# Kernel optimization log

Hardware: AMD Instinct MI355X
Metric: run time of the kernel (lower is better)

Reference implementation:

```python
import jax, jax.numpy as jnp
import numpy as np
from jax import lax

B, L, IN_DIM, D_MODEL = 4, 4096, 256, 512
EXPAND, D_STATE, D_CONV = 2, 16, 4
D_INNER = EXPAND * D_MODEL              # 1024
DT_RANK = (D_MODEL + 15) // 16          # 32 (mamba default: ceil(d_model/16))


def setup_inputs() -> dict:
    key = jax.random.key(0)
    ks = jax.random.split(key, 12)
    s = 0.02
    x = jax.random.normal(ks[0], (B, L, IN_DIM), dtype=jnp.float32)
    # input_proj: nn.Linear(input_dim, d_model) with bias
    w_proj = jax.random.normal(ks[1], (IN_DIM, D_MODEL), dtype=jnp.float32) * s
    b_proj = jnp.zeros((D_MODEL,), dtype=jnp.float32)
    # Mamba in_proj: Linear(d_model, 2*d_inner, bias=False)
    in_w = jax.random.normal(ks[2], (D_MODEL, 2 * D_INNER), dtype=jnp.float32) * s
    # depthwise causal conv1d: weight (d_inner, d_conv), bias (d_inner,)
    conv_w = jax.random.normal(ks[3], (D_INNER, D_CONV), dtype=jnp.float32) * s
    conv_b = jnp.zeros((D_INNER,), dtype=jnp.float32)
    # x_proj: Linear(d_inner, dt_rank + 2*d_state, bias=False)
    xproj_w = jax.random.normal(ks[4], (D_INNER, DT_RANK + 2 * D_STATE), dtype=jnp.float32) * s
    # dt_proj: Linear(dt_rank, d_inner) with bias
    dt_w = jax.random.normal(ks[5], (DT_RANK, D_INNER), dtype=jnp.float32) * s
    dt_b = jax.random.normal(ks[6], (D_INNER,), dtype=jnp.float32) * 0.1
    # A_log init: log(1..d_state) broadcast over d_inner (mamba S4D-real init)
    A_log = jnp.log(jnp.broadcast_to(jnp.arange(1, D_STATE + 1, dtype=jnp.float32), (D_INNER, D_STATE)))
    D_skip = jnp.ones((D_INNER,), dtype=jnp.float32)
    # out_proj: Linear(d_inner, d_model, bias=False)
    out_w = jax.random.normal(ks[7], (D_INNER, D_MODEL), dtype=jnp.float32) * s
    return {"x": x, "w_proj": w_proj, "b_proj": b_proj, "in_w": in_w,
            "conv_w": conv_w, "conv_b": conv_b, "xproj_w": xproj_w,
            "dt_w": dt_w, "dt_b": dt_b, "A_log": A_log, "D_skip": D_skip,
            "out_w": out_w}


def _mamba_forward(x, w_proj, b_proj, in_w, conv_w, conv_b, xproj_w,
                   dt_w, dt_b, A_log, D_skip, out_w):
    silu = jax.nn.silu
    # input projection: [B,L,IN_DIM] -> [B,L,D_MODEL]
    h = x @ w_proj + b_proj
    # in_proj -> split into x-branch and gate z: each [B,L,D_INNER]
    xz = h @ in_w
    u, z = jnp.split(xz, 2, axis=-1)
    # depthwise causal conv1d over L
    u_c = jnp.transpose(u, (0, 2, 1))                       # [B,E,L]
    u_c = jnp.pad(u_c, ((0, 0), (0, 0), (D_CONV - 1, 0)))   # causal left-pad
    u_c = lax.conv_general_dilated(
        u_c, conv_w[:, None, :], window_strides=(1,), padding='VALID',
        dimension_numbers=('NCH', 'OIH', 'NCH'), feature_group_count=D_INNER)
    u = silu(jnp.transpose(u_c, (0, 2, 1)) + conv_b)         # [B,L,E]
    # input-dependent dt, B, C
    x_dbl = u @ xproj_w                                      # [B,L,dt_rank+2N]
    dt, Bm, Cm = jnp.split(x_dbl, [DT_RANK, DT_RANK + D_STATE], axis=-1)
    dt = jax.nn.softplus(dt @ dt_w + dt_b)                   # [B,L,E]
    A = -jnp.exp(A_log)                                      # [E,N]
    # selective scan over time (carry h: [B,E,N])
    def step(hs, inp):
        dt_t, B_t, C_t, u_t = inp                            # (B,E),(B,N),(B,N),(B,E)
        dA = jnp.exp(dt_t[..., None] * A)                    # [B,E,N]
        hs = dA * hs + (dt_t * u_t)[..., None] * B_t[:, None, :]
        y_t = jnp.einsum('ben,bn->be', hs, C_t)
        return hs, y_t
    xs = (jnp.transpose(dt, (1, 0, 2)), jnp.transpose(Bm, (1, 0, 2)),
          jnp.transpose(Cm, (1, 0, 2)), jnp.transpose(u, (1, 0, 2)))
    h0 = jnp.zeros((B, D_INNER, D_STATE), dtype=u.dtype)
    _, ys = lax.scan(step, h0, xs)                           # [L,B,E]
    y = jnp.transpose(ys, (1, 0, 2)) + u * D_skip            # [B,L,E]
    y = y * silu(z)
    out = y @ out_w                                          # [B,L,D_MODEL]
    return out.mean(axis=1)                                  # [B,D_MODEL]


def reference(x, w_proj, b_proj, in_w, conv_w, conv_b, xproj_w,
              dt_w, dt_b, A_log, D_skip, out_w):
    return _mamba_forward(x, w_proj, b_proj, in_w, conv_w, conv_b, xproj_w,
                          dt_w, dt_b, A_log, D_skip, out_w)
```

## Files before the change

### kernel.cpp

```cpp
#include <hip/hip_runtime.h>
#include <cstdint>
#include <cstddef>


#define B_    4
#define L_    4096
#define M_    (B_ * L_)
#define DIN   256
#define DM    512
#define DI    1024
#define NS    16
#define RK    32
#define XD    64
#define TCH   64
#define NCH   (L_ / TCH)
#define NCHAN (B_ * DI)

#define L2E   1.44269504088896f
#define LN2   0.69314718055995f

typedef __bf16 bf16_t;
typedef bf16_t bf16x8 __attribute__((ext_vector_type(8)));
typedef float  f32x4  __attribute__((ext_vector_type(4)));

static __device__ __forceinline__ float fexp2(float x)  { return __builtin_amdgcn_exp2f(x); }
static __device__ __forceinline__ float frcp(float x)   { return __builtin_amdgcn_rcpf(x); }
static __device__ __forceinline__ float flog2(float x)  { return __builtin_amdgcn_logf(x); }
static __device__ __forceinline__ float fsigmoid(float x) {
  return frcp(1.f + fexp2(-x * L2E));
}

static __device__ __forceinline__ unsigned short f32_to_bf16_rne(float f) {
  unsigned u = __float_as_uint(f);
  u += 0x7fffu + ((u >> 16) & 1u);
  return (unsigned short)(u >> 16);
}
static __device__ __forceinline__ float bf16_to_f32(unsigned short h) {
  return __uint_as_float(((unsigned)h) << 16);
}

typedef __attribute__((address_space(1))) const unsigned int ga_u32;
typedef __attribute__((address_space(3))) unsigned int ls_u32;
static __device__ __forceinline__ void glds16(const void* g, void* l) {
  __builtin_amdgcn_global_load_lds((ga_u32*)g, (ls_u32*)l, 16, 0, 0);
}

static __device__ __forceinline__ void tsp_tile(
    const float* __restrict__ W, int K, int N, int kt, int nt,
    unsigned short* __restrict__ Thi, unsigned short* __restrict__ Tlo,
    float (*tile)[33], int tx, int ty)
{
#pragma unroll
  for (int i = ty; i < 32; i += 8)
    tile[i][tx] = W[(size_t)(kt + i) * N + nt + tx];
  __syncthreads();
#pragma unroll
  for (int i = ty; i < 32; i += 8) {
    float f = tile[tx][i];
    unsigned short hi = f32_to_bf16_rne(f);
    size_t o = (size_t)(nt + i) * K + kt + tx;
    Thi[o] = hi;
    Tlo[o] = f32_to_bf16_rne(f - bf16_to_f32(hi));
  }
}

__global__ __launch_bounds__(256) void prep_k(
    const float* __restrict__ x, const float* __restrict__ w_proj,
    const float* __restrict__ b_proj, const float* __restrict__ in_w,
    const float* __restrict__ xproj_w, const float* __restrict__ dt_w,
    float* __restrict__ xdbl, float* __restrict__ sacc,
    float* __restrict__ outbuf, float* __restrict__ bias2,
    unsigned short* __restrict__ inT_hi, unsigned short* __restrict__ inT_lo,
    unsigned short* __restrict__ xpT_hi, unsigned short* __restrict__ xpT_lo,
    unsigned short* __restrict__ dtT_hi, unsigned short* __restrict__ dtT_lo,
    unsigned short* __restrict__ wp_hi,  unsigned short* __restrict__ wp_lo,
    unsigned short* __restrict__ x_bf)
{
  __shared__ float tile[32][33];
  const int blk = blockIdx.x, tid = threadIdx.x;
  const int tx = tid & 31, ty = tid >> 5;
  const float4 z4 = make_float4(0.f, 0.f, 0.f, 0.f);

  if (blk < 1024) {
    ((float4*)xdbl)[blk * 256 + tid] = z4;
  } else if (blk == 1024) {
#pragma unroll
    for (int j = 0; j < 4; ++j) ((float4*)sacc)[tid + 256 * j] = z4;
  } else if (blk == 1025) {
#pragma unroll
    for (int j = 0; j < 2; ++j) ((float4*)outbuf)[tid + 256 * j] = z4;
  } else if (blk < 1034) {
    int n = (blk - 1026) * 256 + tid;
    float acc = 0.f;
    for (int k = 0; k < DM; ++k)
      acc = fmaf(b_proj[k], in_w[(size_t)k * (2 * DI) + n], acc);
    bias2[n] = acc;
  } else if (blk < 2058) {
    int t = blk - 1034;
    tsp_tile(in_w, DM, 2 * DI, (t & 15) * 32, (t >> 4) * 32,
             inT_hi, inT_lo, tile, tx, ty);
  } else if (blk < 2122) {
    int t = blk - 2058;
    tsp_tile(xproj_w, DI, XD, (t & 31) * 32, (t >> 5) * 32,
             xpT_hi, xpT_lo, tile, tx, ty);
  } else if (blk < 2154) {
    int t = blk - 2122;
    tsp_tile(dt_w, RK, DI, 0, t * 32, dtT_hi, dtT_lo, tile, tx, ty);
  } else if (blk < 2282) {
    int i = (blk - 2154) * 256 + tid;
    float4 v = *(const float4*)(w_proj + (size_t)i * 4);
    unsigned short h0 = f32_to_bf16_rne(v.x), h1 = f32_to_bf16_rne(v.y);
    unsigned short h2 = f32_to_bf16_rne(v.z), h3 = f32_to_bf16_rne(v.w);
    *(ushort4*)(wp_hi + (size_t)i * 4) = make_ushort4(h0, h1, h2, h3);
    *(ushort4*)(wp_lo + (size_t)i * 4) =
        make_ushort4(f32_to_bf16_rne(v.x - bf16_to_f32(h0)),
                     f32_to_bf16_rne(v.y - bf16_to_f32(h1)),
                     f32_to_bf16_rne(v.z - bf16_to_f32(h2)),
                     f32_to_bf16_rne(v.w - bf16_to_f32(h3)));
  } else {
    int i = (blk - 2282) * 256 + tid;
    float4 v = *(const float4*)(x + (size_t)i * 4);
    *(ushort4*)(x_bf + (size_t)i * 4) =
        make_ushort4(f32_to_bf16_rne(v.x), f32_to_bf16_rne(v.y),
                     f32_to_bf16_rne(v.z), f32_to_bf16_rne(v.w));
  }
}

template<int OUTMODE>
__global__ __launch_bounds__(256) void gemm_ps3(
    const unsigned short* __restrict__ Ahi, const unsigned short* __restrict__ Alo,
    const unsigned short* __restrict__ Bhi, const unsigned short* __restrict__ Blo,
    const float* __restrict__ bias, void* __restrict__ O1, void* __restrict__ O2,
    int M, int N, int K, int ldc, int splitN)
{
  constexpr int SST = (OUTMODE == 1) ? 16384 : 12288;
  __shared__ __align__(16) unsigned short ls[2 * SST];

  const int tid = threadIdx.x, wave = tid >> 6, lane = tid & 63;
  const int r = lane & 15, kq = lane >> 4;
  const int bm0 = blockIdx.y * 128, bn0 = blockIdx.x * 128;
  const int wm = (wave >> 1) * 4, wn = (wave & 1) * 4;
  const int s0 = wave * 2;

  const unsigned short* gAh = Ahi + (size_t)(bm0 + s0 * 16 + r) * K + kq * 8;
  const unsigned short* gAl = (OUTMODE == 1)
      ? Alo + (size_t)(bm0 + s0 * 16 + r) * K + kq * 8 : nullptr;
  const unsigned short* gBh = Bhi + (size_t)(bn0 + s0 * 16 + r) * K + kq * 8;
  const unsigned short* gBl = Blo + (size_t)(bn0 + s0 * 16 + r) * K + kq * 8;
  const size_t rowK16 = (size_t)16 * K;

  f32x4 acc[4][4];
#pragma unroll
  for (int i = 0; i < 4; ++i)
#pragma unroll
    for (int j = 0; j < 4; ++j) acc[i][j] = 0.f;

#define PS3_STAGE(S)                                                          \
  {                                                                           \
    unsigned short* l = ls + (S) * SST;                                       \
    glds16(gAh,          l + s0 * 512);                                       \
    glds16(gAh + rowK16, l + (s0 + 1) * 512);                                 \
    glds16(gBh,          l + 4096 + s0 * 512);                                \
    glds16(gBh + rowK16, l + 4096 + (s0 + 1) * 512);                          \
    glds16(gBl,          l + 8192 + s0 * 512);                                \
    glds16(gBl + rowK16, l + 8192 + (s0 + 1) * 512);                          \
    if constexpr (OUTMODE == 1) {                                             \
      glds16(gAl,          l + 12288 + s0 * 512);                             \
      glds16(gAl + rowK16, l + 12288 + (s0 + 1) * 512);                       \
    }                                                                         \
    gAh += 32; gBh += 32; gBl += 32;                                          \
    if constexpr (OUTMODE == 1) gAl += 32;                                    \
  }

  const int T = K >> 5;
  PS3_STAGE(0);
  for (int t = 0; t < T; ++t) {
    __syncthreads();
    if (t + 1 < T) PS3_STAGE((t + 1) & 1);
    const unsigned short* l = ls + (t & 1) * SST;
    const unsigned short* lA0 = l;
    const unsigned short* lB0 = l + 4096;
    const unsigned short* lB1 = l + 8192;
    const unsigned short* lA1 = l + 12288;
    bf16x8 ah[4], al[4];
#pragma unroll
    for (int i = 0; i < 4; ++i) {
      ah[i] = *(const bf16x8*)&lA0[(wm + i) * 512 + lane * 8];
      if constexpr (OUTMODE == 1)
        al[i] = *(const bf16x8*)&lA1[(wm + i) * 512 + lane * 8];
    }
#pragma unroll
    for (int j = 0; j < 4; ++j) {
      bf16x8 bh = *(const bf16x8*)&lB0[(wn + j) * 512 + lane * 8];
      bf16x8 bl = *(const bf16x8*)&lB1[(wn + j) * 512 + lane * 8];
#pragma unroll
      for (int i = 0; i < 4; ++i) {
        acc[i][j] = __builtin_amdgcn_mfma_f32_16x16x32_bf16(ah[i], bh, acc[i][j], 0, 0, 0);
        acc[i][j] = __builtin_amdgcn_mfma_f32_16x16x32_bf16(ah[i], bl, acc[i][j], 0, 0, 0);
        if constexpr (OUTMODE == 1)
          acc[i][j] = __builtin_amdgcn_mfma_f32_16x16x32_bf16(al[i], bh, acc[i][j], 0, 0, 0);
      }
    }
  }
#undef PS3_STAGE
  __syncthreads();

  if constexpr (OUTMODE == 2) {
    float* esc = (float*)ls + wave * 1088;
    const bool isz = (bn0 >= splitN);
    unsigned short* obase = isz ? ((unsigned short*)O2 + bn0 - splitN)
                                : ((unsigned short*)O1 + bn0);
    const int cb = (wave & 1) * 64;
    const int rb = (wave >> 1) * 64;
    float bv[4];
#pragma unroll
    for (int j = 0; j < 4; ++j)
      bv[j] = bias ? bias[bn0 + cb + j * 16 + r] : 0.f;
#pragma unroll
    for (int i = 0; i < 4; ++i) {
#pragma unroll
      for (int j = 0; j < 4; ++j)
#pragma unroll
        for (int rr = 0; rr < 4; ++rr) {
          float v = acc[i][j][rr] + bv[j];
          if (isz) v = v * fsigmoid(v);
          esc[(kq * 4 + rr) * 68 + j * 16 + r] = v;
        }
#pragma unroll
      for (int c = 0; c < 4; ++c) {
        int f = c * 64 + lane;
        int rl = f >> 4, c4 = (f & 15) * 4;
        float4 v = *(const float4*)&esc[rl * 68 + c4];
        ushort4 o = make_ushort4(f32_to_bf16_rne(v.x), f32_to_bf16_rne(v.y),
                                 f32_to_bf16_rne(v.z), f32_to_bf16_rne(v.w));
        *(ushort4*)&obase[(size_t)(bm0 + rb + i * 16 + rl) * ldc + cb + c4] = o;
      }
    }
  } else {
    unsigned short* Chi = (unsigned short*)O1;
    unsigned short* Clo = (unsigned short*)O2;
#pragma unroll
    for (int j = 0; j < 4; ++j) {
      int gc = bn0 + (wn + j) * 16 + r;
#pragma unroll
      for (int i = 0; i < 4; ++i) {
        int gr = bm0 + (wm + i) * 16 + kq * 4;
#pragma unroll
        for (int rr = 0; rr < 4; ++rr) {
          float v = acc[i][j][rr];
          unsigned short hi = f32_to_bf16_rne(v);
          Chi[(size_t)(gr + rr) * ldc + gc] = hi;
          Clo[(size_t)(gr + rr) * ldc + gc] = f32_to_bf16_rne(v - bf16_to_f32(hi));
        }
      }
    }
  }
}

__global__ __launch_bounds__(256) void gemm_dt(
    const float* __restrict__ xdbl, const unsigned short* __restrict__ Bhi,
    const unsigned short* __restrict__ Blo, const float* __restrict__ dtb,
    float* __restrict__ dtv)
{
  __shared__ __align__(16) unsigned short lAhi[128 * 32];
  __shared__ __align__(16) unsigned short lBhi[128 * 32];
  __shared__ __align__(16) unsigned short lBlo[128 * 32];
  const int tid = threadIdx.x, wave = tid >> 6, lane = tid & 63;
  const int r = lane & 15, kq = lane >> 4;
  const int bm0 = blockIdx.y * 128, bn0 = blockIdx.x * 128;
  const int wm = (wave >> 1) * 4, wn = (wave & 1) * 4;

  {
    const int row = tid >> 1, c0 = (tid & 1) * 16;
    const float* src = xdbl + (size_t)(bm0 + row) * XD + c0;
#pragma unroll
    for (int j = 0; j < 4; ++j) {
      float4 v = *(const float4*)(src + 4 * j);
      *(ushort4*)&lAhi[row * 32 + c0 + 4 * j] =
          make_ushort4(f32_to_bf16_rne(v.x), f32_to_bf16_rne(v.y),
                       f32_to_bf16_rne(v.z), f32_to_bf16_rne(v.w));
    }
    const uint4* sbh = (const uint4*)(Bhi + (size_t)bn0 * 32);
    const uint4* sbl = (const uint4*)(Blo + (size_t)bn0 * 32);
    ((uint4*)lBhi)[tid] = sbh[tid];
    ((uint4*)lBhi)[tid + 256] = sbh[tid + 256];
    ((uint4*)lBlo)[tid] = sbl[tid];
    ((uint4*)lBlo)[tid + 256] = sbl[tid + 256];
  }
  __syncthreads();

  f32x4 acc[4][4];
#pragma unroll
  for (int i = 0; i < 4; ++i)
#pragma unroll
    for (int j = 0; j < 4; ++j) acc[i][j] = 0.f;

  bf16x8 ah[4];
#pragma unroll
  for (int i = 0; i < 4; ++i)
    ah[i] = *(const bf16x8*)&lAhi[((wm + i) * 16 + r) * 32 + kq * 8];
#pragma unroll
  for (int j = 0; j < 4; ++j) {
    int col = ((wn + j) * 16 + r) * 32 + kq * 8;
    bf16x8 bh = *(const bf16x8*)&lBhi[col];
    bf16x8 bl = *(const bf16x8*)&lBlo[col];
#pragma unroll
    for (int i = 0; i < 4; ++i) {
      acc[i][j] = __builtin_amdgcn_mfma_f32_16x16x32_bf16(ah[i], bh, acc[i][j], 0, 0, 0);
      acc[i][j] = __builtin_amdgcn_mfma_f32_16x16x32_bf16(ah[i], bl, acc[i][j], 0, 0, 0);
    }
  }
#pragma unroll
  for (int j = 0; j < 4; ++j) {
    int gc = bn0 + (wn + j) * 16 + r;
    float bv = dtb[gc];
#pragma unroll
    for (int i = 0; i < 4; ++i) {
      int gr = bm0 + (wm + i) * 16 + kq * 4;
#pragma unroll
      for (int rr = 0; rr < 4; ++rr) {
        float a = acc[i][j][rr] + bv;
        float t = fexp2(-fabsf(a) * L2E);
        dtv[(size_t)(gr + rr) * DI + gc] =
            fmaxf(a, 0.f) + flog2(1.f + t) * LN2;
      }
    }
  }
}

__global__ __launch_bounds__(256) void gemm_splitk(
    const unsigned short* __restrict__ Ahi,
    const unsigned short* __restrict__ Bhi, const unsigned short* __restrict__ Blo,
    float* __restrict__ Cacc, int M, int N, int K, int kslice)
{
  __shared__ __align__(16) unsigned short lsm[2][3 * 2048];
  const int tid  = threadIdx.x;
  const int wave = tid >> 6, lane = tid & 63;
  const int r = lane & 15, kq = lane >> 4;
  const int am = (wave >> 1) * 2, bn = (wave & 1) * 2;
  const int bm0 = blockIdx.y * 64, bn0 = blockIdx.x * 64;
  const int kz  = blockIdx.z;
  const int kbeg = kz * kslice;

  const unsigned short* gA  = Ahi + (size_t)(bm0 + wave * 16 + r) * K + kbeg + kq * 8;
  const unsigned short* gBh = Bhi + (size_t)(bn0 + wave * 16 + r) * K + kbeg + kq * 8;
  const unsigned short* gBl = Blo + (size_t)(bn0 + wave * 16 + r) * K + kbeg + kq * 8;

  f32x4 acc[2][2];
#pragma unroll
  for (int i = 0; i < 2; ++i)
#pragma unroll
    for (int j = 0; j < 2; ++j) acc[i][j] = 0.f;

#define SK_STAGE(S)                                 \
  {                                                 \
    unsigned short* l = &lsm[S][0];                 \
    glds16(gA,  l + wave * 512);                    \
    glds16(gBh, l + 2048 + wave * 512);             \
    glds16(gBl, l + 4096 + wave * 512);             \
    gA += 32; gBh += 32; gBl += 32;                 \
  }

  const int T = kslice >> 5;
  SK_STAGE(0);
  for (int t = 0; t < T; ++t) {
    __syncthreads();
    if (t + 1 < T) SK_STAGE((t + 1) & 1);
    const unsigned short* l = &lsm[t & 1][0];
    bf16x8 ah[2];
#pragma unroll
    for (int i = 0; i < 2; ++i)
      ah[i] = *(const bf16x8*)&l[(am + i) * 512 + lane * 8];
#pragma unroll
    for (int j = 0; j < 2; ++j) {
      bf16x8 bh = *(const bf16x8*)&l[2048 + (bn + j) * 512 + lane * 8];
      bf16x8 bl = *(const bf16x8*)&l[4096 + (bn + j) * 512 + lane * 8];
#pragma unroll
      for (int i = 0; i < 2; ++i) {
        acc[i][j] = __builtin_amdgcn_mfma_f32_16x16x32_bf16(ah[i], bh, acc[i][j], 0, 0, 0);
        acc[i][j] = __builtin_amdgcn_mfma_f32_16x16x32_bf16(ah[i], bl, acc[i][j], 0, 0, 0);
      }
    }
  }
#undef SK_STAGE
#pragma unroll
  for (int j = 0; j < 2; ++j) {
    int gc = bn0 + (bn + j) * 16 + r;
#pragma unroll
    for (int i = 0; i < 2; ++i) {
      int gr = bm0 + (am + i) * 16 + kq * 4;
#pragma unroll
      for (int rr = 0; rr < 4; ++rr)
        atomicAdd(&Cacc[(size_t)(gr + rr) * N + gc], acc[i][j][rr]);
    }
  }
}

__global__ __launch_bounds__(256) void conv_silu(
    const unsigned short* __restrict__ u, const float* __restrict__ cw,
    const float* __restrict__ cb, unsigned short* __restrict__ uc_hi)
{
  int idx = blockIdx.x * 256 + threadIdx.x;
  int e4 = idx & (DI / 4 - 1);
  int m  = idx >> 8;
  int t  = m & (L_ - 1);
  int e  = e4 << 2;
  const float* wp = cw + e * 4;
  float4 wa = *(const float4*)(wp);
  float4 wb = *(const float4*)(wp + 4);
  float4 wc = *(const float4*)(wp + 8);
  float4 wd = *(const float4*)(wp + 12);
  float4 acc = *(const float4*)(cb + e);
  const unsigned short* ur = u + (size_t)m * DI + e;
#pragma unroll
  for (int k = 0; k < 4; ++k) {
    if (t - 3 + k >= 0) {
      ushort4 uv = *(const ushort4*)(ur + (ptrdiff_t)(k - 3) * DI);
      acc.x = fmaf(bf16_to_f32(uv.x), ((const float*)&wa)[k], acc.x);
      acc.y = fmaf(bf16_to_f32(uv.y), ((const float*)&wb)[k], acc.y);
      acc.z = fmaf(bf16_to_f32(uv.z), ((const float*)&wc)[k], acc.z);
      acc.w = fmaf(bf16_to_f32(uv.w), ((const float*)&wd)[k], acc.w);
    }
  }
  float o0 = acc.x * fsigmoid(acc.x);
  float o1 = acc.y * fsigmoid(acc.y);
  float o2 = acc.z * fsigmoid(acc.z);
  float o3 = acc.w * fsigmoid(acc.w);
  *(ushort4*)(uc_hi + (size_t)m * DI + e) =
      make_ushort4(f32_to_bf16_rne(o0), f32_to_bf16_rne(o1),
                   f32_to_bf16_rne(o2), f32_to_bf16_rne(o3));
}

__global__ __launch_bounds__(256) void scan_fused(
    const float* __restrict__ dtv, const unsigned short* __restrict__ uch,
    const float* __restrict__ xdbl, const float* __restrict__ A_log,
    const unsigned short* __restrict__ gate, const float* __restrict__ Dsk,
    float* __restrict__ Pbuf, float* __restrict__ Hbuf,
    float* __restrict__ Gbuf, float* __restrict__ sacc)
{
  const int l = threadIdx.x & 63;
  const int wave = __builtin_amdgcn_readfirstlane(threadIdx.x >> 6);
  const int cw = wave >> 1, sp = wave & 1;
  const int chan = blockIdx.x * 128 + cw * 64 + l;
  const int e = chan & (DI - 1);
  const int b = blockIdx.x >> 3;
  const int chunk = blockIdx.y;

  float Aef[8];
#pragma unroll
  for (int j = 0; j < 8; ++j)
    Aef[j] = -__expf(A_log[e * NS + sp * 8 + j]) * L2E;
  const float dAef = Aef[1] - Aef[0];
  const float Dv = (sp == 0) ? Dsk[e] : 0.f;

  const size_t m0 = (size_t)b * L_ + (size_t)chunk * TCH;
  const float* pd = dtv  + m0 * DI + e;
  const unsigned short* pu = uch + m0 * DI + e;
  const unsigned short* pg = gate + m0 * DI + e;
  const float* px = xdbl + m0 * XD + RK + sp * 8;

  float h[8], cp[8], g[8];
#pragma unroll
  for (int j = 0; j < 8; ++j) { h[j] = 0.f; cp[j] = 1.f; g[j] = 0.f; }
  float ssum = 0.f, asum = 0.f;

#define SCAN_STEP(PD, PU, PG, PX)                                            \
  {                                                                          \
    float a  = *(PD);                                                        \
    float uu = bf16_to_f32(*(PU));                                           \
    float gt = bf16_to_f32(*(PG));                                           \
    float4 b0 = *(const float4*)(PX);                                        \
    float4 b1 = *(const float4*)((PX) + 4);                                  \
    float4 c0 = *(const float4*)((PX) + 2 * NS);                             \
    float4 c1 = *(const float4*)((PX) + 2 * NS + 4);                         \
    float du = a * uu;                                                       \
    asum += a;                                                               \
    float dA = fexp2(a * Aef[0]);                                            \
    float qr = fexp2(a * dAef);                                              \
    float bb[8] = {b0.x, b0.y, b0.z, b0.w, b1.x, b1.y, b1.z, b1.w};          \
    float cc[8] = {c0.x, c0.y, c0.z, c0.w, c1.x, c1.y, c1.z, c1.w};          \
    float y = 0.f;                                                           \
    _Pragma("unroll")                                                        \
    for (int j = 0; j < 8; ++j) {                                            \
      h[j] = fmaf(dA, h[j], du * bb[j]);                                     \
      cp[j] *= dA;                                                           \
      g[j] = fmaf(gt * cp[j], cc[j], g[j]);                                  \
      y = fmaf(h[j], cc[j], y);                                              \
      dA *= qr;                                                              \
    }                                                                        \
    ssum = fmaf(gt, fmaf(uu, Dv, y), ssum);                                  \
  }

  for (int t = 0; t < TCH; t += 4) {
    SCAN_STEP(pd,          pu,          pg,          px);
    SCAN_STEP(pd + DI,     pu + DI,     pg + DI,     px + XD);
    SCAN_STEP(pd + 2 * DI, pu + 2 * DI, pg + 2 * DI, px + 2 * XD);
    SCAN_STEP(pd + 3 * DI, pu + 3 * DI, pg + 3 * DI, px + 3 * XD);
    pd += 4 * DI; pu += 4 * DI; pg += 4 * DI; px += 4 * XD;
  }
#undef SCAN_STEP

  size_t base = ((size_t)chunk * NS + sp * 8) * NCHAN + chan;
#pragma unroll
  for (int j = 0; j < 8; ++j) {
    Pbuf[base + (size_t)j * NCHAN] = fexp2(Aef[j] * asum);
    Hbuf[base + (size_t)j * NCHAN] = h[j];
    Gbuf[base + (size_t)j * NCHAN] = g[j];
  }
  atomicAdd(&sacc[chan], ssum);
}

__global__ __launch_bounds__(256) void scan_compose(
    const float* __restrict__ Pbuf, const float* __restrict__ Hbuf,
    const float* __restrict__ Gbuf, float* __restrict__ sacc)
{
  int idx = blockIdx.x * 256 + threadIdx.x;
  int chan = idx & (NCHAN - 1);
  int n = idx >> 12;
  float h0 = 0.f, acc = 0.f;
  size_t o = (size_t)n * NCHAN + chan;
  const size_t step = (size_t)NS * NCHAN;
  for (int c = 0; c < NCH; ++c, o += step) {
    acc = fmaf(Gbuf[o], h0, acc);
    h0 = fmaf(Pbuf[o], h0, Hbuf[o]);
  }
  atomicAdd(&sacc[chan], acc);
}

__global__ __launch_bounds__(64) void out_proj_k(
    const float* __restrict__ s, const float* __restrict__ ow,
    float* __restrict__ out)
{
  int d = blockIdx.x * 64 + threadIdx.x;
  int b = blockIdx.y;
  int e0 = blockIdx.z * 128;
  const float* sb = s + b * DI;
  float acc = 0.f;
  for (int e = e0; e < e0 + 128; ++e)
    acc = fmaf(sb[e], ow[(size_t)e * DM + d], acc);
  atomicAdd(&out[b * DM + d], acc * (1.f / (float)L_));
}

extern "C" void kernel_launch(void* const* d_in, const int* in_sizes, int n_in,
                              void* d_out, int out_size, void* d_ws, size_t ws_size,
                              hipStream_t stream)
{
  const float* x      = (const float*)d_in[0];
  const float* w_proj = (const float*)d_in[1];
  const float* b_proj = (const float*)d_in[2];
  const float* in_w   = (const float*)d_in[3];
  const float* conv_w = (const float*)d_in[4];
  const float* conv_b = (const float*)d_in[5];
  const float* xproj_w= (const float*)d_in[6];
  const float* dt_w   = (const float*)d_in[7];
  const float* dt_b   = (const float*)d_in[8];
  const float* A_log  = (const float*)d_in[9];
  const float* D_skip = (const float*)d_in[10];
  const float* out_w  = (const float*)d_in[11];

  float* ws   = (float*)d_ws;
  float* bufA = ws;
  unsigned short* bufZ16 = (unsigned short*)(bufA + (size_t)M_ * DI);
  unsigned short* bufC16 = bufZ16 + (size_t)M_ * DI;
  float* xdbl = (float*)(bufC16 + (size_t)M_ * DI);
  float* Pb   = xdbl + (size_t)M_ * XD;
  float* Hb   = Pb   + (size_t)NCH * NS * NCHAN;
  float* Gb   = Hb   + (size_t)NCH * NS * NCHAN;
  float* sacc = Gb   + (size_t)NCH * NS * NCHAN;
  unsigned short* inT_hi = (unsigned short*)(sacc + NCHAN);
  unsigned short* inT_lo = inT_hi + (size_t)2 * DI * DM;
  unsigned short* wp_hi  = inT_lo + (size_t)2 * DI * DM;
  unsigned short* wp_lo  = wp_hi  + (size_t)DIN * DM;
  unsigned short* w12_hi = wp_lo  + (size_t)DIN * DM;
  unsigned short* w12_lo = w12_hi + (size_t)2 * DI * DIN;
  unsigned short* xpT_hi = w12_lo + (size_t)2 * DI * DIN;
  unsigned short* xpT_lo = xpT_hi + (size_t)XD * DI;
  unsigned short* dtT_hi = xpT_lo + (size_t)XD * DI;
  unsigned short* dtT_lo = dtT_hi + (size_t)DI * RK;
  float* bias2 = (float*)(dtT_lo + (size_t)DI * RK);

  unsigned short* x_bf    = bufC16;
  unsigned short* u_bf    = (unsigned short*)bufA;
  unsigned short* gate_bf = bufZ16;
  unsigned short* uc_hi   = bufC16;
  float* dtv  = bufA;

  prep_k<<<6378, 256, 0, stream>>>(
      x, w_proj, b_proj, in_w, xproj_w, dt_w,
      xdbl, sacc, (float*)d_out, bias2,
      inT_hi, inT_lo, xpT_hi, xpT_lo, dtT_hi, dtT_lo, wp_hi, wp_lo, x_bf);
  gemm_ps3<1><<<dim3(DIN / 128, 2 * DI / 128), 256, 0, stream>>>(
      inT_hi, inT_lo, wp_hi, wp_lo, nullptr, w12_hi, w12_lo,
      2 * DI, DIN, DM, DIN, DIN);
  gemm_ps3<2><<<dim3(2 * DI / 128, M_ / 128), 256, 0, stream>>>(
      x_bf, nullptr, w12_hi, w12_lo, bias2, u_bf, gate_bf, M_, 2 * DI, DIN, DI, DI);
  conv_silu<<<(M_ * DI / 4) / 256, 256, 0, stream>>>(
      u_bf, conv_w, conv_b, uc_hi);
  gemm_splitk<<<dim3(1, M_ / 64, 4), 256, 0, stream>>>(
      uc_hi, xpT_hi, xpT_lo, xdbl, M_, XD, DI, DI / 4);
  gemm_dt<<<dim3(DI / 128, M_ / 128), 256, 0, stream>>>(
      xdbl, dtT_hi, dtT_lo, dt_b, dtv);
  scan_fused<<<dim3(NCHAN / 128, NCH), 256, 0, stream>>>(
      dtv, uc_hi, xdbl, A_log, gate_bf, D_skip, Pb, Hb, Gb, sacc);
  scan_compose<<<(NCHAN * NS) / 256, 256, 0, stream>>>(Pb, Hb, Gb, sacc);
  out_proj_k<<<dim3(DM / 64, B_, DI / 128), 64, 0, stream>>>(
      sacc, out_w, (float*)d_out);
}
```

Measured before the change: 342.3 us.

## Triple-buffer LDS in GEMM kernels with partial vmcnt waits and MFMA priority

New measurement: 339.2 us. Within noise of the previous version (-0.9%).

```diff
diff --git a/kernel.cpp b/kernel.cpp
--- a/kernel.cpp
+++ b/kernel.cpp
@@ -134,7 +134,7 @@
     int M, int N, int K, int ldc, int splitN)
 {
   constexpr int SST = (OUTMODE == 1) ? 16384 : 12288;
-  __shared__ __align__(16) unsigned short ls[2 * SST];
+  __shared__ __align__(16) unsigned short ls[3 * SST];
 
   const int tid = threadIdx.x, wave = tid >> 6, lane = tid & 63;
   const int r = lane & 15, kq = lane >> 4;
@@ -174,10 +174,21 @@
 
   const int T = K >> 5;
   PS3_STAGE(0);
+  PS3_STAGE(1);
+  int slc = 0;
+  int sls = 2;
   for (int t = 0; t < T; ++t) {
-    __syncthreads();
-    if (t + 1 < T) PS3_STAGE((t + 1) & 1);
-    const unsigned short* l = ls + (t & 1) * SST;
+    if (t != T - 1) {
+      if constexpr (OUTMODE == 1)
+        asm volatile("s_waitcnt vmcnt(8) lgkmcnt(0)" ::: "memory");
+      else
+        asm volatile("s_waitcnt vmcnt(6) lgkmcnt(0)" ::: "memory");
+    } else {
+      asm volatile("s_waitcnt vmcnt(0) lgkmcnt(0)" ::: "memory");
+    }
+    asm volatile("s_barrier" ::: "memory");
+    if (t + 2 < T) PS3_STAGE(sls);
+    const unsigned short* l = ls + slc * SST;
     const unsigned short* lA0 = l;
     const unsigned short* lB0 = l + 4096;
     const unsigned short* lB1 = l + 8192;
@@ -189,6 +200,7 @@
       if constexpr (OUTMODE == 1)
         al[i] = *(const bf16x8*)&lA1[(wm + i) * 512 + lane * 8];
     }
+    __builtin_amdgcn_s_setprio(1);
 #pragma unroll
     for (int j = 0; j < 4; ++j) {
       bf16x8 bh = *(const bf16x8*)&lB0[(wn + j) * 512 + lane * 8];
@@ -201,6 +213,9 @@
           acc[i][j] = __builtin_amdgcn_mfma_f32_16x16x32_bf16(al[i], bh, acc[i][j], 0, 0, 0);
       }
     }
+    __builtin_amdgcn_s_setprio(0);
+    slc = (slc == 2) ? 0 : slc + 1;
+    sls = (sls == 2) ? 0 : sls + 1;
   }
 #undef PS3_STAGE
   __syncthreads();
@@ -333,7 +348,7 @@
     const unsigned short* __restrict__ Bhi, const unsigned short* __restrict__ Blo,
     float* __restrict__ Cacc, int M, int N, int K, int kslice)
 {
-  __shared__ __align__(16) unsigned short lsm[2][3 * 2048];
+  __shared__ __align__(16) unsigned short lsm[3][3 * 2048];
   const int tid  = threadIdx.x;
   const int wave = tid >> 6, lane = tid & 63;
   const int r = lane & 15, kq = lane >> 4;
@@ -363,14 +378,21 @@
 
   const int T = kslice >> 5;
   SK_STAGE(0);
+  SK_STAGE(1);
+  int slc = 0, sls = 2;
   for (int t = 0; t < T; ++t) {
-    __syncthreads();
-    if (t + 1 < T) SK_STAGE((t + 1) & 1);
-    const unsigned short* l = &lsm[t & 1][0];
+    if (t != T - 1)
+      asm volatile("s_waitcnt vmcnt(3) lgkmcnt(0)" ::: "memory");
+    else
+      asm volatile("s_waitcnt vmcnt(0) lgkmcnt(0)" ::: "memory");
+    asm volatile("s_barrier" ::: "memory");
+    if (t + 2 < T) SK_STAGE(sls);
+    const unsigned short* l = &lsm[slc][0];
     bf16x8 ah[2];
 #pragma unroll
     for (int i = 0; i < 2; ++i)
       ah[i] = *(const bf16x8*)&l[(am + i) * 512 + lane * 8];
+    __builtin_amdgcn_s_setprio(1);
 #pragma unroll
     for (int j = 0; j < 2; ++j) {
       bf16x8 bh = *(const bf16x8*)&l[2048 + (bn + j) * 512 + lane * 8];
@@ -381,6 +403,9 @@
         acc[i][j] = __builtin_amdgcn_mfma_f32_16x16x32_bf16(ah[i], bl, acc[i][j], 0, 0, 0);
       }
     }
+    __builtin_amdgcn_s_setprio(0);
+    slc = (slc == 2) ? 0 : slc + 1;
+    sls = (sls == 2) ? 0 : sls + 1;
   }
 #undef SK_STAGE
 #pragma unroll
```
